# Optimization experiments

Hardware: AMD Instinct MI355X
Metric: run time of the kernel (lower is better)

The kernel has to match this reference:

```python
import jax, jax.numpy as jnp
import numpy as np

LN_EPS = 1e-12  # default nn.LayerNorm eps used by the HF ViT config


def setup_inputs() -> dict:
    key = jax.random.key(0)
    ks = jax.random.split(key, 6)
    B, H, S, D = 2, 12, 197, 768
    Hd = D // H
    hidden_states = jax.random.normal(ks[0], (B, S, D), jnp.float32)
    # attention probs: softmax-normalized over last axis for realism
    logits = jax.random.normal(ks[1], (B, H, S, S), jnp.float32)
    attention_probs = jax.nn.softmax(logits, axis=-1)
    value_layer = jax.random.normal(ks[2], (B, H, S, Hd), jnp.float32)
    dense_weight = jax.random.normal(ks[3], (D, D), jnp.float32) * 0.02
    ln_weight = jax.random.uniform(ks[4], (D,), jnp.float32, 0.5, 1.5)
    pre_ln_states = jax.random.normal(ks[5], (B, S, D), jnp.float32)
    return {
        'hidden_states': hidden_states,
        'attention_probs': attention_probs,
        'value_layer': value_layer,
        'dense_weight': dense_weight,
        'ln_weight': ln_weight,
        'pre_ln_states': pre_ln_states,
    }


def _norm(x):
    return jnp.linalg.norm(x, axis=-1)


def _diag_bsd(x):
    # torch.diagonal(x, dim1=1, dim2=2).permute(0,2,1): (b,k,s,d)->(b,s,d)
    return jnp.transpose(jnp.diagonal(x, axis1=1, axis2=2), (0, 2, 1))


def reference(hidden_states, attention_probs, value_layer, dense_weight, ln_weight, pre_ln_states):
    B, S, D = hidden_states.shape
    H = attention_probs.shape[1]
    Hd = D // H
    # dense.weight.view(all_head, H, Hd)
    dw = dense_weight.reshape(D, H, Hd)
    transformed = jnp.einsum('bhsv,dhv->bhsd', value_layer, dw)          # (B,H,S,D)
    weighted = jnp.einsum('bhks,bhsd->bhksd', attention_probs, transformed)  # (B,H,S,S,D)
    weighted_norm = _norm(weighted)                                       # (B,H,S,S)
    summed = weighted.sum(axis=1)                                         # (B,S,S,D)
    summed_norm = _norm(summed)
    residual = jnp.einsum('sk,bsd->bskd', jnp.eye(S, dtype=hidden_states.dtype), hidden_states)
    residual_weighted = summed + residual                                 # (B,S,S,D)
    residual_weighted_norm = _norm(residual_weighted)
    # LayerNorm decomposition: variance from pre_ln_states, mean per-component
    mean = pre_ln_states.mean(-1, keepdims=True)                          # (B,S,1)
    var = ((pre_ln_states - mean) ** 2).mean(-1, keepdims=True)[:, :, None]  # (B,S,1,1)
    each_mean = residual_weighted.mean(-1, keepdims=True)
    normalized = (residual_weighted - each_mean) / jnp.sqrt(var + LN_EPS)
    post_ln = normalized * ln_weight                                      # (B,S,S,D)
    post_ln_norm = _norm(post_ln)
    # mixing ratios
    def mixing_ratio(x):
        preserving = _diag_bsd(x)
        mixing = x.sum(axis=2) - preserving
        pn, mn = _norm(preserving), _norm(mixing)
        return mn / (mn + pn)
    attn_mix = mixing_ratio(summed)
    attnres_mix = mixing_ratio(residual_weighted)
    attnresln_mix = mixing_ratio(post_ln)
    return (weighted_norm, summed_norm, residual_weighted_norm, post_ln_norm,
            post_ln, attn_mix, attnres_mix, attnresln_mix)
```

## Files before the change

### kernel.cpp

```cpp
#include <hip/hip_runtime.h>
#include <cstdint>

#define S_ 197
#define D_ 768
#define H_ 12
#define B_ 2
#define SS_ (S_*S_)

#define O_WN   0
#define O_SN   931416
#define O_RWN  1009034
#define O_PLNN 1086652
#define O_PLN  1164270
#define O_AM   60774894
#define O_ARM  60775288
#define O_ARLM 60775682

#define WS_T2   0
#define WS_TN   3631104
#define WS_ACC  3635832
#define WS_WT   3635832
#define WS_SMU  4846200
#define WS_MUI  4847776
#define WS_P3   4848170

#define I_T 4
#define NC 4
#define JCM 50

__device__ __forceinline__ float wred64(float v) {
#pragma unroll
  for (int off = 32; off > 0; off >>= 1) v += __shfl_xor(v, off);
  return v;
}

__device__ __forceinline__ void load12(const float* __restrict__ p, float t[12]) {
  const float4* q = (const float4*)p;
  float4 a = q[0], b = q[1], c = q[2];
  t[0]=a.x; t[1]=a.y; t[2]=a.z; t[3]=a.w;
  t[4]=b.x; t[5]=b.y; t[6]=b.z; t[7]=b.w;
  t[8]=c.x; t[9]=c.y; t[10]=c.z; t[11]=c.w;
}

__global__ __launch_bounds__(256) void kTranspose(const float* __restrict__ in,
                                                  float* __restrict__ outp) {
  __shared__ float tile[32][33];
  int x = blockIdx.x*32 + threadIdx.x;
  int y = blockIdx.y*32 + threadIdx.y;
#pragma unroll
  for (int k = 0; k < 32; k += 8) tile[threadIdx.y+k][threadIdx.x] = in[(y+k)*D_ + x];
  __syncthreads();
  x = blockIdx.y*32 + threadIdx.x;
  y = blockIdx.x*32 + threadIdx.y;
#pragma unroll
  for (int k = 0; k < 32; k += 8) outp[(y+k)*D_ + x] = tile[threadIdx.x][threadIdx.y+k];
}

#define TST 8
__global__ __launch_bounds__(256) void kTransform(const float* __restrict__ V,
                                                  const float* __restrict__ Wt,
                                                  float* __restrict__ T2,
                                                  float* __restrict__ tnorm) {
  int blk = blockIdx.x;
  int xcd = blk & 7; int slot = blk >> 3;
  int bh = xcd*3 + (slot % 3);
  int st = slot / 3;
  int h = bh % H_; int b = bh / H_;
  int s0 = st*TST; int ns = min(TST, S_ - s0);
  __shared__ float vt[TST*64];
  __shared__ float red[4][TST];
  int t = threadIdx.x;
  const float* Vbase = V + ((size_t)bh*S_ + s0)*64;
  for (int e = t; e < ns*64; e += 256) vt[e] = Vbase[e];
  __syncthreads();
  float acc2[TST];
#pragma unroll
  for (int s = 0; s < TST; s++) acc2[s] = 0.f;
  for (int g = 0; g < 3; g++) {
    int d = t + g*256;
    float acc[TST];
#pragma unroll
    for (int s = 0; s < TST; s++) acc[s] = 0.f;
    const float* wp = Wt + (size_t)h*64*D_ + d;
#pragma unroll 8
    for (int v = 0; v < 64; v++) {
      float wv = wp[(size_t)v*D_];
#pragma unroll
      for (int s = 0; s < TST; s++) acc[s] = fmaf(vt[s*64+v], wv, acc[s]);
    }
    for (int s = 0; s < ns; s++) {
      T2[((size_t)(b*S_ + s0+s)*H_ + h)*D_ + d] = acc[s];
      acc2[s] = fmaf(acc[s], acc[s], acc2[s]);
    }
  }
  int lane = t & 63, wq = t >> 6;
#pragma unroll
  for (int s = 0; s < TST; s++) {
    float v = wred64(acc2[s]);
    if (lane == 0) red[wq][s] = v;
  }
  __syncthreads();
  if (t < ns) {
    float v = red[0][t] + red[1][t] + red[2][t] + red[3][t];
    tnorm[bh*S_ + s0 + t] = sqrtf(v);
  }
}

__global__ __launch_bounds__(512) void kMain(const float* __restrict__ attn,
                                             const float* __restrict__ hs,
                                             const float* __restrict__ lnw,
                                             const float* __restrict__ preln,
                                             const float* __restrict__ T2,
                                             const float* __restrict__ tnorm,
                                             float* __restrict__ outp,
                                             float* __restrict__ wsAccS,
                                             float* __restrict__ wsSmu,
                                             float* __restrict__ wsMui,
                                             float* __restrict__ wsP) {
  int blk = blockIdx.x;
  int xcd = blk & 7; int it = blk >> 3;
  int b = xcd >> 2;  int c = xcd & 3;
  int i0 = it * I_T;
  int jc0 = (c == 3) ? 149 : c*50;
  int jcE = (c == 0) ? 50 : (c == 1) ? 100 : (c == 2) ? 149 : 197;
  int jcW = jcE - jc0;
  int ni = min(I_T, S_ - i0);
  int tid = threadIdx.x;
  int lane = tid & 63, wv = tid >> 6;
  int dbase = lane * 12;

  __shared__ float ash[H_*I_T*JCM];
  __shared__ float tnl[H_*JCM];
  __shared__ float sAcc[I_T*D_];
  __shared__ float sSmu[8*I_T];

  int tot = H_*I_T*jcW;
  for (int e = tid; e < tot; e += 512) {
    int hh = e / (I_T*jcW); int rem = e - hh*(I_T*jcW);
    int ii = rem / jcW; int jj = rem - ii*jcW;
    int iG = i0 + ii;
    float v = 0.f;
    if (iG < S_) v = attn[((size_t)(b*H_ + hh)*S_ + iG)*S_ + (jc0 + jj)];
    ash[(hh*I_T + ii)*JCM + jj] = v;
  }
  for (int e = tid; e < H_*jcW; e += 512) {
    int hh = e / jcW; int jj = e - hh*jcW;
    tnl[hh*JCM + jj] = tnorm[(b*H_ + hh)*S_ + jc0 + jj];
  }

  float w_[12];
  load12(lnw + dbase, w_);
  float w2s_l = 0.f;
#pragma unroll
  for (int m = 0; m < 12; m++) w2s_l = fmaf(w_[m], w_[m], w2s_l);
  float w2sum = wred64(w2s_l);

  float istd[I_T];
#pragma unroll
  for (int ii = 0; ii < I_T; ii++) {
    int iG = i0 + ii;
    istd[ii] = 0.f;
    if (iG < S_) {
      float x[12];
      load12(preln + (size_t)(b*S_ + iG)*D_ + dbase, x);
      float sx = 0.f, sx2 = 0.f;
#pragma unroll
      for (int m = 0; m < 12; m++) { sx += x[m]; sx2 = fmaf(x[m], x[m], sx2); }
      sx = wred64(sx); sx2 = wred64(sx2);
      float mu = sx * (1.0f/768.0f);
      float var = sx2 * (1.0f/768.0f) - mu*mu;
      istd[ii] = 1.0f / sqrtf(var + 1e-12f);
    }
  }

  float accS[I_T][12];
#pragma unroll
  for (int ii = 0; ii < I_T; ii++)
#pragma unroll
    for (int m = 0; m < 12; m++) accS[ii][m] = 0.f;
  float smu[I_T] = {0.f, 0.f, 0.f, 0.f};

  __syncthreads();

  for (int j = jc0 + wv; j < jcE; j += 8) {
    int jj = j - jc0;
    const float* tb = T2 + (size_t)(b*S_ + j)*H_*D_ + dbase;
    float s[I_T][12];
#pragma unroll
    for (int ii = 0; ii < I_T; ii++)
#pragma unroll
      for (int m = 0; m < 12; m++) s[ii][m] = 0.f;
#pragma unroll 2
    for (int h = 0; h < H_; h++) {
      float t[12];
      load12(tb + h*D_, t);
#pragma unroll
      for (int ii = 0; ii < I_T; ii++) {
        float ah = ash[(h*I_T + ii)*JCM + jj];
#pragma unroll
        for (int m = 0; m < 12; m++) s[ii][m] = fmaf(ah, t[m], s[ii][m]);
      }
    }
#pragma unroll
    for (int ii = 0; ii < I_T; ii++) {
      int iG = i0 + ii;
      if (iG < S_) {
        bool isDiag = (j == iG);
        float rw[12];
        if (isDiag) {
          float hh[12];
          load12(hs + (size_t)(b*S_ + iG)*D_ + dbase, hh);
#pragma unroll
          for (int m = 0; m < 12; m++) rw[m] = s[ii][m] + hh[m];
        } else {
#pragma unroll
          for (int m = 0; m < 12; m++) rw[m] = s[ii][m];
        }
        float ls2 = 0.f, lrw = 0.f, lrw2 = 0.f, lrww2 = 0.f, lrw2w2 = 0.f;
#pragma unroll
        for (int m = 0; m < 12; m++) {
          ls2 = fmaf(s[ii][m], s[ii][m], ls2);
          lrw += rw[m];
          float t1 = rw[m] * w_[m];
          lrww2 = fmaf(t1, w_[m], lrww2);
          lrw2 = fmaf(rw[m], rw[m], lrw2);
          lrw2w2 = fmaf(t1, t1, lrw2w2);
        }
        ls2 = wred64(ls2); lrw = wred64(lrw); lrw2 = wred64(lrw2);
        lrww2 = wred64(lrww2); lrw2w2 = wred64(lrw2w2);
        float mu = lrw * (1.0f/768.0f);
        float q = fmaf(mu*mu, w2sum, fmaf(-2.0f*mu, lrww2, lrw2w2));
        q = fmaxf(q, 0.f);
        float plnn = istd[ii] * sqrtf(q);
        int oIdx = (b*S_ + iG)*S_ + j;
        if (lane == 0) {
          outp[O_SN + oIdx] = sqrtf(ls2);
          outp[O_RWN + oIdx] = sqrtf(lrw2);
          outp[O_PLNN + oIdx] = plnn;
        }
        float* po = outp + O_PLN + (size_t)oIdx*D_ + dbase;
        float a = istd[ii];
        float p[12];
#pragma unroll
        for (int m = 0; m < 12; m++) p[m] = (rw[m] - mu) * a * w_[m];
        *(float2*)po        = make_float2(p[0], p[1]);
        *(float4*)(po + 2)  = make_float4(p[2], p[3], p[4], p[5]);
        *(float4*)(po + 6)  = make_float4(p[6], p[7], p[8], p[9]);
        *(float2*)(po + 10) = make_float2(p[10], p[11]);
        smu[ii] += mu;
        if (isDiag) {
          if (lane == 0) {
            wsMui[b*S_ + iG] = mu;
            wsP[(b*S_ + iG)*3 + 0] = ls2;
            wsP[(b*S_ + iG)*3 + 1] = lrw2;
            wsP[(b*S_ + iG)*3 + 2] = q;
          }
        } else {
#pragma unroll
          for (int m = 0; m < 12; m++) accS[ii][m] += s[ii][m];
        }
      }
    }
  }

  if (lane == 0) {
#pragma unroll
    for (int ii = 0; ii < I_T; ii++) sSmu[wv*I_T + ii] = smu[ii];
  }
  for (int rr = 0; rr < 8; rr++) {
    __syncthreads();
    if (wv == rr) {
#pragma unroll
      for (int ii = 0; ii < I_T; ii++) {
        if (ii < ni) {
#pragma unroll
          for (int m = 0; m < 12; m++) {
            int a = ii*D_ + dbase + m;
            sAcc[a] = (rr == 0) ? accS[ii][m] : (sAcc[a] + accS[ii][m]);
          }
        }
      }
    }
  }
  __syncthreads();
  for (int e = tid; e < ni*192; e += 512) {
    int ii = e / 192; int d4 = (e % 192) * 4;
    float4 v = *(float4*)&sAcc[ii*D_ + d4];
    *(float4*)(wsAccS + (size_t)((b*S_ + i0 + ii)*NC + c)*D_ + d4) = v;
  }
  if (tid < ni) {
    float ss = 0.f;
#pragma unroll
    for (int wq = 0; wq < 8; wq++) ss += sSmu[wq*I_T + tid];
    wsSmu[(b*S_ + i0 + tid)*NC + c] = ss;
  }
  int totW = H_*ni*jcW;
  for (int e = tid; e < totW; e += 512) {
    int hh = e / (ni*jcW); int rem = e - hh*(ni*jcW);
    int ii = rem / jcW; int jj = rem - ii*jcW;
    int iG = i0 + ii;
    outp[O_WN + ((size_t)(b*H_ + hh)*S_ + iG)*S_ + jc0 + jj] =
        fabsf(ash[(hh*I_T + ii)*JCM + jj]) * tnl[hh*JCM + jj];
  }
}

__global__ __launch_bounds__(256) void kMixing(const float* __restrict__ wsAccS,
                                               const float* __restrict__ wsSmu,
                                               const float* __restrict__ wsMui,
                                               const float* __restrict__ wsP,
                                               const float* __restrict__ lnw,
                                               float* __restrict__ outp) {
  int bi = blockIdx.x;
  int t = threadIdx.x;
  float Smu = wsSmu[bi*4] + wsSmu[bi*4+1] + wsSmu[bi*4+2] + wsSmu[bi*4+3];
  float mui = wsMui[bi];
  float dmu = Smu - mui;
  float mS = 0.f, mP = 0.f;
#pragma unroll
  for (int g = 0; g < 3; g++) {
    int d = t + g*256;
    float mix = wsAccS[((size_t)bi*4 + 0)*D_ + d] + wsAccS[((size_t)bi*4 + 1)*D_ + d]
              + wsAccS[((size_t)bi*4 + 2)*D_ + d] + wsAccS[((size_t)bi*4 + 3)*D_ + d];
    float w = lnw[d];
    mS = fmaf(mix, mix, mS);
    float mp = w * (mix - dmu);
    mP = fmaf(mp, mp, mP);
  }
  __shared__ float red[4][2];
  int lane = t & 63, wv = t >> 6;
  mS = wred64(mS); mP = wred64(mP);
  if (lane == 0) { red[wv][0] = mS; red[wv][1] = mP; }
  __syncthreads();
  if (t == 0) {
    float a0 = 0.f, a1 = 0.f;
#pragma unroll
    for (int k = 0; k < 4; k++) { a0 += red[k][0]; a1 += red[k][1]; }
    float mn = sqrtf(a0), mnp = sqrtf(a1);
    float pn   = sqrtf(wsP[bi*3 + 0]);
    float pnrw = sqrtf(wsP[bi*3 + 1]);
    float pnp  = sqrtf(wsP[bi*3 + 2]);
    outp[O_AM   + bi] = mn / (mn + pn);
    outp[O_ARM  + bi] = mn / (mn + pnrw);
    outp[O_ARLM + bi] = mnp / (mnp + pnp);
  }
}

extern "C" void kernel_launch(void* const* d_in, const int* in_sizes, int n_in,
                              void* d_out, int out_size, void* d_ws, size_t ws_size,
                              hipStream_t stream) {
  const float* hs    = (const float*)d_in[0];
  const float* attn  = (const float*)d_in[1];
  const float* V     = (const float*)d_in[2];
  const float* W     = (const float*)d_in[3];
  const float* lnw   = (const float*)d_in[4];
  const float* preln = (const float*)d_in[5];
  float* out = (float*)d_out;
  float* ws  = (float*)d_ws;

  kTranspose<<<dim3(24,24), dim3(32,8), 0, stream>>>(W, ws + WS_WT);
  kTransform<<<dim3(600), dim3(256), 0, stream>>>(V, ws + WS_WT, ws + WS_T2, ws + WS_TN);
  kMain<<<dim3(400), dim3(512), 0, stream>>>(attn, hs, lnw, preln, ws + WS_T2, ws + WS_TN,
                                             out, ws + WS_ACC, ws + WS_SMU, ws + WS_MUI, ws + WS_P3);
  kMixing<<<dim3(B_*S_), dim3(256), 0, stream>>>(ws + WS_ACC, ws + WS_SMU, ws + WS_MUI, ws + WS_P3,
                                                 lnw, out);
}
```

Measured before the change: 370.4 us.

## Split key range into two chunks and use 768-thread blocks in main kernel

The main kernel's key (j) range is now split into two chunks of 99 instead of four of about 50. Blocks grow from 8 to 12 wavefronts and the grid shrinks from 400 to 200 blocks, with the block-to-XCD mapping changed to match. The mixing kernel and the workspace offsets shrink to reduce only two partial sums per row. Fewer blocks means each attention/T2 tile is shared over a longer j range and there is less partial-sum traffic, at the cost of fewer blocks to fill the GPU and more shared memory per block.

```diff
diff --git a/kernel.cpp b/kernel.cpp
--- a/kernel.cpp
+++ b/kernel.cpp
@@ -20,13 +20,14 @@
 #define WS_TN   3631104
 #define WS_ACC  3635832
 #define WS_WT   3635832
-#define WS_SMU  4846200
-#define WS_MUI  4847776
-#define WS_P3   4848170
+#define WS_SMU  4241016
+#define WS_MUI  4241804
+#define WS_P3   4242198
 
 #define I_T 4
-#define NC 4
-#define JCM 50
+#define NIT 50
+#define NC 2
+#define JC 99
 
 __device__ __forceinline__ float wred64(float v) {
 #pragma unroll
@@ -106,7 +107,7 @@
   }
 }
 
-__global__ __launch_bounds__(512) void kMain(const float* __restrict__ attn,
+__global__ __launch_bounds__(768) void kMain(const float* __restrict__ attn,
                                              const float* __restrict__ hs,
                                              const float* __restrict__ lnw,
                                              const float* __restrict__ preln,
@@ -118,34 +119,36 @@
                                              float* __restrict__ wsMui,
                                              float* __restrict__ wsP) {
   int blk = blockIdx.x;
-  int xcd = blk & 7; int it = blk >> 3;
-  int b = xcd >> 2;  int c = xcd & 3;
+  int xcd = blk & 7; int slot = blk >> 3;
+  int b = (xcd >> 2) & 1;
+  int c = (xcd >> 1) & 1;
+  int it = slot*2 + (xcd & 1);
   int i0 = it * I_T;
-  int jc0 = (c == 3) ? 149 : c*50;
-  int jcE = (c == 0) ? 50 : (c == 1) ? 100 : (c == 2) ? 149 : 197;
+  int jc0 = c * JC;
+  int jcE = min(jc0 + JC, S_);
   int jcW = jcE - jc0;
   int ni = min(I_T, S_ - i0);
   int tid = threadIdx.x;
   int lane = tid & 63, wv = tid >> 6;
   int dbase = lane * 12;
 
-  __shared__ float ash[H_*I_T*JCM];
-  __shared__ float tnl[H_*JCM];
+  __shared__ float ash[H_*I_T*JC];
+  __shared__ float tnl[H_*JC];
   __shared__ float sAcc[I_T*D_];
-  __shared__ float sSmu[8*I_T];
+  __shared__ float sSmu[12*I_T];
 
   int tot = H_*I_T*jcW;
-  for (int e = tid; e < tot; e += 512) {
+  for (int e = tid; e < tot; e += 768) {
     int hh = e / (I_T*jcW); int rem = e - hh*(I_T*jcW);
     int ii = rem / jcW; int jj = rem - ii*jcW;
     int iG = i0 + ii;
     float v = 0.f;
     if (iG < S_) v = attn[((size_t)(b*H_ + hh)*S_ + iG)*S_ + (jc0 + jj)];
-    ash[(hh*I_T + ii)*JCM + jj] = v;
-  }
-  for (int e = tid; e < H_*jcW; e += 512) {
+    ash[(hh*I_T + ii)*JC + jj] = v;
+  }
+  for (int e = tid; e < H_*jcW; e += 768) {
     int hh = e / jcW; int jj = e - hh*jcW;
-    tnl[hh*JCM + jj] = tnorm[(b*H_ + hh)*S_ + jc0 + jj];
+    tnl[hh*JC + jj] = tnorm[(b*H_ + hh)*S_ + jc0 + jj];
   }
 
   float w_[12];
@@ -182,7 +185,7 @@
 
   __syncthreads();
 
-  for (int j = jc0 + wv; j < jcE; j += 8) {
+  for (int j = jc0 + wv; j < jcE; j += 12) {
     int jj = j - jc0;
     const float* tb = T2 + (size_t)(b*S_ + j)*H_*D_ + dbase;
     float s[I_T][12];
@@ -196,7 +199,7 @@
       load12(tb + h*D_, t);
 #pragma unroll
       for (int ii = 0; ii < I_T; ii++) {
-        float ah = ash[(h*I_T + ii)*JCM + jj];
+        float ah = ash[(h*I_T + ii)*JC + jj];
 #pragma unroll
         for (int m = 0; m < 12; m++) s[ii][m] = fmaf(ah, t[m], s[ii][m]);
       }
@@ -267,7 +270,7 @@
 #pragma unroll
     for (int ii = 0; ii < I_T; ii++) sSmu[wv*I_T + ii] = smu[ii];
   }
-  for (int rr = 0; rr < 8; rr++) {
+  for (int rr = 0; rr < 12; rr++) {
     __syncthreads();
     if (wv == rr) {
 #pragma unroll
@@ -283,24 +286,24 @@
     }
   }
   __syncthreads();
-  for (int e = tid; e < ni*192; e += 512) {
-    int ii = e / 192; int d4 = (e % 192) * 4;
+  if (tid < ni*192) {
+    int ii = tid / 192; int d4 = (tid % 192) * 4;
     float4 v = *(float4*)&sAcc[ii*D_ + d4];
     *(float4*)(wsAccS + (size_t)((b*S_ + i0 + ii)*NC + c)*D_ + d4) = v;
   }
   if (tid < ni) {
     float ss = 0.f;
 #pragma unroll
-    for (int wq = 0; wq < 8; wq++) ss += sSmu[wq*I_T + tid];
+    for (int wq = 0; wq < 12; wq++) ss += sSmu[wq*I_T + tid];
     wsSmu[(b*S_ + i0 + tid)*NC + c] = ss;
   }
   int totW = H_*ni*jcW;
-  for (int e = tid; e < totW; e += 512) {
+  for (int e = tid; e < totW; e += 768) {
     int hh = e / (ni*jcW); int rem = e - hh*(ni*jcW);
     int ii = rem / jcW; int jj = rem - ii*jcW;
     int iG = i0 + ii;
     outp[O_WN + ((size_t)(b*H_ + hh)*S_ + iG)*S_ + jc0 + jj] =
-        fabsf(ash[(hh*I_T + ii)*JCM + jj]) * tnl[hh*JCM + jj];
+        fabsf(ash[(hh*I_T + ii)*JC + jj]) * tnl[hh*JC + jj];
   }
 }
 
@@ -312,15 +315,14 @@
                                                float* __restrict__ outp) {
   int bi = blockIdx.x;
   int t = threadIdx.x;
-  float Smu = wsSmu[bi*4] + wsSmu[bi*4+1] + wsSmu[bi*4+2] + wsSmu[bi*4+3];
+  float Smu = wsSmu[bi*2] + wsSmu[bi*2 + 1];
   float mui = wsMui[bi];
   float dmu = Smu - mui;
   float mS = 0.f, mP = 0.f;
 #pragma unroll
   for (int g = 0; g < 3; g++) {
     int d = t + g*256;
-    float mix = wsAccS[((size_t)bi*4 + 0)*D_ + d] + wsAccS[((size_t)bi*4 + 1)*D_ + d]
-              + wsAccS[((size_t)bi*4 + 2)*D_ + d] + wsAccS[((size_t)bi*4 + 3)*D_ + d];
+    float mix = wsAccS[((size_t)bi*2 + 0)*D_ + d] + wsAccS[((size_t)bi*2 + 1)*D_ + d];
     float w = lnw[d];
     mS = fmaf(mix, mix, mS);
     float mp = w * (mix - dmu);
@@ -359,8 +361,8 @@
 
   kTranspose<<<dim3(24,24), dim3(32,8), 0, stream>>>(W, ws + WS_WT);
   kTransform<<<dim3(600), dim3(256), 0, stream>>>(V, ws + WS_WT, ws + WS_T2, ws + WS_TN);
-  kMain<<<dim3(400), dim3(512), 0, stream>>>(attn, hs, lnw, preln, ws + WS_T2, ws + WS_TN,
-                                             out, ws + WS_ACC, ws + WS_SMU, ws + WS_MUI, ws + WS_P3);
+  kMain<<<dim3(B_*NIT*NC), dim3(768), 0, stream>>>(attn, hs, lnw, preln, ws + WS_T2, ws + WS_TN,
+                                                   out, ws + WS_ACC, ws + WS_SMU, ws + WS_MUI, ws + WS_P3);
   kMixing<<<dim3(B_*S_), dim3(256), 0, stream>>>(ws + WS_ACC, ws + WS_SMU, ws + WS_MUI, ws + WS_P3,
                                                  lnw, out);
 }
```

Result: faster. 347.2 us (-6.3%).
